# Performance work log

Measured on AMD Instinct MI355X. Metric: run time of the kernel, lower is better.

The kernel has to match this reference:

```python
import jax, jax.numpy as jnp
import numpy as np

TEMP = 0.05
EPS_SOFTMAX = 1e-6
EPS_LOG = 1e-6


def setup_inputs() -> dict:
    key = jax.random.key(0)
    k1, k2, k3, k4, k5 = jax.random.split(key, 5)
    B, F, N, C = 256, 128, 200000, 1000
    inputs = jax.random.normal(k1, (B, F), dtype=jnp.float32)
    inputs_s = jax.random.normal(k2, (B, F), dtype=jnp.float32)
    features = jax.random.normal(k3, (N, F), dtype=jnp.float32)
    # memory banks are kept L2-normalized (see MB.backward renorm)
    features = features / jnp.linalg.norm(features, axis=1, keepdims=True)
    labels = jax.random.randint(k4, (N,), 0, C, dtype=jnp.int64)
    indexes = jax.random.randint(k5, (B,), 0, N, dtype=jnp.int64)
    return {"inputs": inputs, "inputs_s": inputs_s, "features": features,
            "labels": labels, "indexes": indexes, "k": 10, "num_classes": C}


def reference(inputs, inputs_s, features, labels, indexes, k, num_classes):
    B = inputs.shape[0]
    N = features.shape[0]
    # features is a buffer (no grad in torch); MB backward also treats it as constant
    feats = jax.lax.stop_gradient(features)

    # MB.forward: inputs @ features.T, then /temp  -> [B, N]
    inputs_out = (inputs @ feats.T) / TEMP

    # local similarity [B, B]
    local = inputs @ inputs_s.T
    # topk neighbors in the bank, gather + per-sample bmm, sum over k -> [B, 1]
    _, nb_idx = jax.lax.top_k(inputs_out, k)          # [B, k]
    nb_ftr = feats[nb_idx]                             # [B, k, F]
    _local = jnp.einsum('bf,bkf->b', inputs, nb_ftr)[:, None]  # [B, 1]
    # (local + _local) masked to diagonal, then /temp
    local = (local + _local) * jnp.eye(B, dtype=local.dtype)
    local = local / TEMP

    targets = labels[indexes]                          # [B]

    # label-bucketed segment reductions -> sim [C, B]
    sim = jax.ops.segment_sum(inputs_out.T, labels, num_segments=num_classes)
    sim = sim + jax.ops.segment_sum(local, targets, num_segments=num_classes)

    nums = jax.ops.segment_sum(jnp.ones((N, 1), jnp.float32), labels,
                               num_segments=num_classes)        # [C, 1]
    nums_help = jax.ops.segment_sum(jnp.ones((B, 1), jnp.float32), targets,
                                    num_segments=num_classes)   # [C, 1]
    nums = nums + (nums_help > 0).astype(jnp.float32) * (k + 1)

    mask = (nums > 0).astype(jnp.float32)              # [C, 1]
    sim = sim / (mask * nums + (1.0 - mask))           # broadcast over B

    # masked softmax over classes, per sample: vec [B, C], mask [1, C]
    vec = sim.T
    m = mask.T                                          # [1, C]
    exps = jnp.exp(vec) * m
    masked_sim = exps / (jnp.sum(exps, axis=1, keepdims=True) + EPS_SOFTMAX)

    logp = jnp.log(masked_sim + EPS_LOG)
    loss = -jnp.mean(logp[jnp.arange(B), targets])
    return loss
```

## Files before the change

### kernel.cpp

```cpp
#include <hip/hip_runtime.h>

#define CMAX 1024
#define BQ 256
#define FQ 128
#define TN 64
#define QCAP 128
#define NBLK_DEF 768

typedef __attribute__((ext_vector_type(8))) short bf16x8;
typedef __attribute__((ext_vector_type(4))) float f32x4;

__device__ __forceinline__ unsigned short f2bf(float f){
  unsigned u = __float_as_uint(f);
  unsigned r = (u + 0x7FFFu + ((u >> 16) & 1u)) >> 16;
  return (unsigned short)r;
}
__device__ __forceinline__ unsigned encf(float f){
  unsigned u = __float_as_uint(f);
  return (u & 0x80000000u) ? ~u : (u | 0x80000000u);
}
__device__ __forceinline__ void ins16(float (&d)[16], float v){
  #pragma unroll
  for (int j = 15; j > 0; --j) d[j] = fminf(d[j-1], fmaxf(v, d[j]));
  d[0] = fmaxf(v, d[0]);
}

__global__ void k_prep(const float* __restrict__ inputs, const float* __restrict__ inputs_s,
                       const int* __restrict__ labels, const int* __restrict__ indexes,
                       unsigned short* __restrict__ inputs_bf,
                       int* __restrict__ cnt, int* __restrict__ numsh,
                       int* __restrict__ targets, float* __restrict__ diag,
                       float* __restrict__ thr, int N)
{
  __shared__ int h[CMAX];
  int t = threadIdx.x;
  for (int c = t; c < CMAX; c += 256) h[c] = 0;
  __syncthreads();
  int idx = blockIdx.x*256 + t;
  int stride = gridDim.x*256;
  for (int n = idx; n < N; n += stride) atomicAdd(&h[labels[n]], 1);
  for (int i = idx; i < BQ*FQ; i += stride) inputs_bf[i] = f2bf(inputs[i]);
  __syncthreads();
  for (int c = t; c < CMAX; c += 256){
    int v = h[c];
    if (v) atomicAdd(&cnt[c], v);
  }
  if (blockIdx.x == 0 && t < BQ){
    int tg = labels[indexes[t]];
    targets[t] = tg;
    atomicAdd(&numsh[tg], 1);
    float s = 0.f, s2 = 0.f;
    const float4* a = (const float4*)(inputs + t*FQ);
    const float4* b = (const float4*)(inputs_s + t*FQ);
    #pragma unroll
    for (int f = 0; f < FQ/4; ++f){
      float4 x = a[f], y = b[f];
      s  += x.x*y.x + x.y*y.y + x.z*y.z + x.w*y.w;
      s2 += x.x*x.x + x.y*x.y + x.z*x.z + x.w*x.w;
    }
    diag[t] = s;
    thr[t] = 3.05f * sqrtf(s2 * (1.0f/128.0f));
  }
}

__global__ void k_scan(const int* __restrict__ cnt, int* __restrict__ cur,
                       int* __restrict__ pstart, const int* __restrict__ cptr)
{
  __shared__ int s[CMAX];
  int C = cptr[0]; if (C > CMAX) C = CMAX;
  int t = threadIdx.x;
  s[t] = (t < C) ? cnt[t] : 0;
  __syncthreads();
  for (int off = 1; off < CMAX; off <<= 1){
    int v = s[t] + ((t >= off) ? s[t - off] : 0);
    __syncthreads();
    s[t] = v;
    __syncthreads();
  }
  if (t < C){
    int e = s[t] - cnt[t];
    cur[t] = e;
    pstart[t] = e;
  }
  if (t == C-1) pstart[C] = s[t];
}

__global__ void k_scatter(const int* __restrict__ labels, int* __restrict__ cur,
                          int* __restrict__ sorted_idx, int* __restrict__ sorted_cls, int N)
{
  int idx = blockIdx.x*blockDim.x + threadIdx.x;
  int stride = gridDim.x*blockDim.x;
  for (int n = idx; n < N; n += stride){
    int c = labels[n];
    int pos = atomicAdd(&cur[c], 1);
    sorted_idx[pos] = n;
    sorted_cls[pos] = c;
  }
}

__global__ __launch_bounds__(256, 3) void k_main(
    const float* __restrict__ feats,
    const int* __restrict__ sorted_idx,
    const int* __restrict__ sorted_cls,
    const unsigned short* __restrict__ inputs_bf,
    const float* __restrict__ thr,
    const int* __restrict__ pstart,
    float* __restrict__ sim,
    float* __restrict__ topk_ws,
    const int* __restrict__ cptr,
    int N, int nblk)
{
  __shared__ unsigned short fl[TN*FQ];
  __shared__ unsigned q_lds[4][QCAP];
  __shared__ int qn_lds[4];

  const int t = threadIdx.x;
  const int lane = t & 63;
  const int w = t >> 6;
  const int c16 = lane & 15;
  const int g = lane >> 4;
  const int g4 = g * 4;
  const int b0 = w * 64;
  const int rowoff = t >> 2;
  const int q = t & 3;

  float d[16];
  #pragma unroll
  for (int i2 = 0; i2 < 16; ++i2) d[i2] = -INFINITY;

  int C = cptr[0]; if (C > CMAX) C = CMAX;
  const int j = blockIdx.x;
  const int Tj  = (int)(((long long)j * N) / nblk);
  const int Tj1 = (int)(((long long)(j+1) * N) / nblk);
  int lo = 0, hi = C;
  while (lo < hi){ int mid = (lo+hi)>>1; if (pstart[mid] < Tj) lo = mid+1; else hi = mid; }
  const int c_lo = lo;
  hi = C;
  while (lo < hi){ int mid = (lo+hi)>>1; if (pstart[mid] < Tj1) lo = mid+1; else hi = mid; }
  const int c_hi = lo;
  const int e_lo = pstart[c_lo];
  const int e_hi = pstart[c_hi];

  if (e_lo < e_hi){
    float thrs[4];
    #pragma unroll
    for (int bt = 0; bt < 4; ++bt) thrs[bt] = thr[b0 + bt*16 + c16];
    float racc[4] = {0.f, 0.f, 0.f, 0.f};
    if (lane == 0) qn_lds[w] = 0;

    const int nch = (e_hi - e_lo + TN - 1) / TN;

    int myrow = e_lo + rowoff;
    int idx_cur = (myrow < e_hi) ? sorted_idx[myrow] : 0;

    for (int m = 0; m < nch; ++m){
      const int base = e_lo + m*TN;
      const int valid = min(TN, e_hi - base);

      const int nxtrow = myrow + TN;
      const int idx_nxt = ((m + 1 < nch) && (nxtrow < e_hi)) ? sorted_idx[nxtrow] : 0;

      const int mypos = base + lane;
      const int myc  = (mypos < e_hi)     ? sorted_cls[mypos]     : -1;
      const int mync = (mypos + 1 < e_hi) ? sorted_cls[mypos + 1] : -2;

      {
        const bool live = (rowoff < valid);
        const float4* src = (const float4*)(feats + (size_t)idx_cur * FQ);
        #pragma unroll
        for (int jj = 0; jj < 8; ++jj){
          float4 v;
          if (live) v = src[jj*4 + q];
          else { v.x = 0.f; v.y = 0.f; v.z = 0.f; v.w = 0.f; }
          int h0 = (jj*16 + q*4) ^ ((rowoff & 7) << 3);
          ushort4 u;
          u.x = f2bf(v.x); u.y = f2bf(v.y); u.z = f2bf(v.z); u.w = f2bf(v.w);
          *(ushort4*)&fl[rowoff*FQ + h0] = u;
        }
      }
      const unsigned long long bmask = __ballot((lane < valid) && (myc != mync));
      __syncthreads();

      f32x4 acc[4][4];
      #pragma unroll
      for (int nt = 0; nt < 4; ++nt)
        #pragma unroll
        for (int bt = 0; bt < 4; ++bt)
          acc[nt][bt] = (f32x4){0.f, 0.f, 0.f, 0.f};
      #pragma unroll
      for (int ks = 0; ks < 4; ++ks){
        bf16x8 af[4], bfr[4];
        #pragma unroll
        for (int nt = 0; nt < 4; ++nt){
          int r = nt*16 + c16;
          int h = r*FQ + ((ks*32 + g*8) ^ ((r & 7) << 3));
          af[nt] = *(const bf16x8*)&fl[h];
        }
        #pragma unroll
        for (int bt = 0; bt < 4; ++bt){
          int b = b0 + bt*16 + c16;
          bfr[bt] = *(const bf16x8*)&inputs_bf[b*FQ + ks*32 + g*8];
        }
        #pragma unroll
        for (int nt = 0; nt < 4; ++nt)
          #pragma unroll
          for (int bt = 0; bt < 4; ++bt)
            acc[nt][bt] = __builtin_amdgcn_mfma_f32_16x16x32_bf16(af[nt], bfr[bt], acc[nt][bt], 0, 0, 0);
      }

      #pragma unroll
      for (int bt = 0; bt < 4; ++bt){
        float smax = -INFINITY;
        #pragma unroll
        for (int nt = 0; nt < 4; ++nt)
          #pragma unroll
          for (int r = 0; r < 4; ++r)
            smax = fmaxf(smax, acc[nt][bt][r]);
        if (__any(smax > thrs[bt])){
          if (smax > thrs[bt]){
            #pragma unroll
            for (int nt = 0; nt < 4; ++nt)
              #pragma unroll
              for (int r = 0; r < 4; ++r){
                float v = acc[nt][bt][r];
                if (v > thrs[bt]){
                  int pos = atomicAdd(&qn_lds[w], 1);
                  if (pos < QCAP)
                    q_lds[w][pos] = (__float_as_uint(v) & 0xFFFFFF00u) | (unsigned)(bt*16 + c16);
                }
              }
          }
        }
      }

      if (bmask == 0ull){
        #pragma unroll
        for (int bt = 0; bt < 4; ++bt){
          float ss = 0.f;
          #pragma unroll
          for (int nt = 0; nt < 4; ++nt)
            #pragma unroll
            for (int r = 0; r < 4; ++r)
              ss += acc[nt][bt][r];
          ss += __shfl_xor(ss, 16, 64);
          ss += __shfl_xor(ss, 32, 64);
          racc[bt] += ss;
        }
      } else {
        int seglo = 0;
        unsigned long long mm = bmask;
        while (mm){
          const int p = (int)__builtin_ctzll(mm);
          float s4[4];
          #pragma unroll
          for (int bt = 0; bt < 4; ++bt){
            float ss = 0.f;
            #pragma unroll
            for (int nt = 0; nt < 4; ++nt)
              #pragma unroll
              for (int r = 0; r < 4; ++r){
                int n = nt*16 + g4 + r;
                ss += ((n >= seglo) && (n <= p)) ? acc[nt][bt][r] : 0.f;
              }
            ss += __shfl_xor(ss, 16, 64);
            ss += __shfl_xor(ss, 32, 64);
            if (seglo == 0) ss += racc[bt];
            s4[bt] = ss;
          }
          const int c = __shfl(myc, p, 64);
          if (g == 0){
            #pragma unroll
            for (int bt = 0; bt < 4; ++bt)
              sim[(size_t)c*BQ + b0 + bt*16 + c16] = s4[bt];
          }
          seglo = p + 1;
          mm &= mm - 1;
        }
        #pragma unroll
        for (int bt = 0; bt < 4; ++bt){
          float ss = 0.f;
          #pragma unroll
          for (int nt = 0; nt < 4; ++nt)
            #pragma unroll
            for (int r = 0; r < 4; ++r){
              int n = nt*16 + g4 + r;
              ss += (n >= seglo) ? acc[nt][bt][r] : 0.f;
            }
          ss += __shfl_xor(ss, 16, 64);
          ss += __shfl_xor(ss, 32, 64);
          racc[bt] = ss;
        }
      }

      __builtin_amdgcn_wave_barrier();
      asm volatile("s_waitcnt lgkmcnt(0)" ::: "memory");
      int qn = qn_lds[w];
      if (qn > QCAP) qn = QCAP;
      for (int qi = 0; qi < qn; ++qi){
        unsigned pk = q_lds[w][qi];
        if ((int)(pk & 0xFFu) == lane){
          float v = __uint_as_float(pk & 0xFFFFFF00u);
          if (v > d[15]) ins16(d, v);
        }
      }
      __builtin_amdgcn_wave_barrier();
      if (lane == 0) qn_lds[w] = 0;

      idx_cur = idx_nxt;
      myrow = nxtrow;
      __syncthreads();
    }
  }

  #pragma unroll
  for (int i2 = 0; i2 < 16; ++i2)
    topk_ws[((size_t)blockIdx.x*BQ + t)*16 + i2] = d[i2];
}

__global__ void k_merge(const float* __restrict__ topk_ws, int NB,
                        const float* __restrict__ diag, const int* __restrict__ targets,
                        float* __restrict__ sim, const int* __restrict__ kptr)
{
  __shared__ float Ld[4][64][16];
  const int t = threadIdx.x;
  const int lane = t & 63;
  const int w = t >> 6;
  const int b = blockIdx.x*4 + w;

  float d[16];
  #pragma unroll
  for (int j = 0; j < 16; ++j) d[j] = -INFINITY;
  for (int bk = lane; bk < NB; bk += 64){
    const float* src = topk_ws + ((size_t)bk*BQ + b)*16;
    for (int j = 0; j < 16; ++j){
      float v = src[j];
      if (!(v > d[15])) break;
      ins16(d, v);
    }
  }
  #pragma unroll
  for (int j = 0; j < 16; ++j) Ld[w][lane][j] = d[j];
  __syncthreads();
  int kk = kptr[0]; if (kk > 16) kk = 16;
  int h = 0;
  float myhead = Ld[w][lane][0];
  float tops = 0.f;
  for (int p = 0; p < 16; ++p){
    unsigned pk = (encf(myhead) & 0xFFFFFFC0u) | (unsigned)lane;
    #pragma unroll
    for (int s = 32; s > 0; s >>= 1){
      unsigned o = (unsigned)__shfl_xor((int)pk, s, 64);
      pk = (o > pk) ? o : pk;
    }
    int wl = (int)(pk & 63u);
    float val = __shfl(myhead, wl, 64);
    if (p < kk) tops += val;
    if (lane == wl){
      ++h;
      myhead = (h < 16) ? Ld[w][lane][h] : -INFINITY;
    }
  }
  if (lane == 0){
    atomicAdd(&sim[(size_t)targets[b]*BQ + b], diag[b] + tops);
  }
}

__global__ void k_expsum(const float* __restrict__ sim, const int* __restrict__ cnt,
                         const int* __restrict__ numsh, const int* __restrict__ targets,
                         const int* __restrict__ kptr, const int* __restrict__ cptr,
                         float* __restrict__ esum, float* __restrict__ etgt)
{
  int t = threadIdx.x;
  int C = cptr[0]; if (C > CMAX) C = CMAX;
  int kk = kptr[0];
  int tgt = targets[t];
  float local = 0.f;
  const float invT = 20.0f;
  for (int c = blockIdx.x; c < C; c += gridDim.x){
    float nums = (float)cnt[c] + ((numsh[c] > 0) ? (float)(kk + 1) : 0.f);
    float denom = (nums > 0.f) ? nums : 1.f;
    float val = sim[(size_t)c*BQ + t] * invT / denom;
    float e = (nums > 0.f) ? expf(val) : 0.f;
    local += e;
    if (c == tgt) etgt[t] = e;
  }
  atomicAdd(&esum[t], local);
}

__global__ void k_loss(const float* __restrict__ esum, const float* __restrict__ etgt,
                       float* __restrict__ out)
{
  __shared__ float red[BQ];
  int t = threadIdx.x;
  float p = etgt[t] / (esum[t] + 1e-6f);
  float l = -logf(p + 1e-6f);
  red[t] = l;
  __syncthreads();
  for (int off = 128; off > 0; off >>= 1){
    if (t < off) red[t] += red[t + off];
    __syncthreads();
  }
  if (t == 0) out[0] = red[0] / 256.0f;
}

extern "C" void kernel_launch(void* const* d_in, const int* in_sizes, int n_in,
                              void* d_out, int out_size, void* d_ws, size_t ws_size,
                              hipStream_t stream) {
  const float* inputs   = (const float*)d_in[0];
  const float* inputs_s = (const float*)d_in[1];
  const float* feats    = (const float*)d_in[2];
  const int*   labels   = (const int*)d_in[3];
  const int*   indexes  = (const int*)d_in[4];
  const int*   kptr     = (const int*)d_in[5];
  const int*   cptr     = (const int*)d_in[6];
  const int N = in_sizes[3];

  char* ws = (char*)d_ws;
  int*      cnt       = (int*)(ws + 0);
  int*      numsh     = (int*)(ws + 4096);
  float*    esum      = (float*)(ws + 8192);
  float*    etgt      = (float*)(ws + 9216);
  int*      targets   = (int*)(ws + 10240);
  float*    diag      = (float*)(ws + 11264);
  float*    thr       = (float*)(ws + 12288);
  int*      cur       = (int*)(ws + 13312);
  int*      pstart    = (int*)(ws + 17408);
  unsigned short* inputs_bf = (unsigned short*)(ws + 21760);
  float*    sim       = (float*)(ws + 87296);
  int*      sorted_idx = (int*)(ws + 1135872);
  int*      sorted_cls = sorted_idx + N;
  size_t off_topk = (1135872 + 8*(size_t)N + 255) & ~(size_t)255;
  float*    topk      = (float*)(ws + off_topk);

  int nblk = NBLK_DEF;
  long long topk_cap = ((long long)ws_size - (long long)off_topk) / (BQ*16*4);
  if (topk_cap < nblk) nblk = (int)topk_cap;
  if (nblk < 1) nblk = 1;
  int gN = (N + 255) / 256; if (gN > 128) gN = 128; if (gN < 1) gN = 1;

  hipMemsetAsync(ws, 0, 10240, stream);
  k_prep<<<64, 256, 0, stream>>>(inputs, inputs_s, labels, indexes, inputs_bf,
                                 cnt, numsh, targets, diag, thr, N);
  k_scan<<<1, 1024, 0, stream>>>(cnt, cur, pstart, cptr);
  k_scatter<<<gN, 256, 0, stream>>>(labels, cur, sorted_idx, sorted_cls, N);
  k_main<<<nblk, 256, 0, stream>>>(feats, sorted_idx, sorted_cls, inputs_bf, thr,
                                   pstart, sim, topk, cptr, N, nblk);
  k_merge<<<BQ/4, 256, 0, stream>>>(topk, nblk, diag, targets, sim, kptr);
  k_expsum<<<64, 256, 0, stream>>>(sim, cnt, numsh, targets, kptr, cptr, esum, etgt);
  k_loss<<<1, 256, 0, stream>>>(esum, etgt, (float*)d_out);
}
```

Measured before the change: 213.3 us.

## Stage gather indices in LDS and defer top-k queue drain to kernel end

Sorted indices and class IDs for each 64-row chunk are now loaded once into shared memory, with the next chunk prefetched into registers. The feature gather is remapped so 32 threads cover one row with coalesced float4 loads, instead of 4 threads per row. The per-chunk top-k candidate queue drain is removed, and candidates accumulate across all chunks in a queue enlarged from 128 to 512 entries, drained once at the end. This cuts per-iteration serial work but uses more LDS, which may lower occupancy, and risks silently dropping candidates if the queue overflows.

```diff
diff --git a/kernel.cpp b/kernel.cpp
--- a/kernel.cpp
+++ b/kernel.cpp
@@ -4,7 +4,7 @@
 #define BQ 256
 #define FQ 128
 #define TN 64
-#define QCAP 128
+#define QCAP 512
 #define NBLK_DEF 768
 
 typedef __attribute__((ext_vector_type(8))) short bf16x8;
@@ -111,6 +111,8 @@
     int N, int nblk)
 {
   __shared__ unsigned short fl[TN*FQ];
+  __shared__ int idx_s[TN];
+  __shared__ int cls_s[TN + 1];
   __shared__ unsigned q_lds[4][QCAP];
   __shared__ int qn_lds[4];
 
@@ -121,12 +123,10 @@
   const int g = lane >> 4;
   const int g4 = g * 4;
   const int b0 = w * 64;
-  const int rowoff = t >> 2;
-  const int q = t & 3;
-
-  float d[16];
-  #pragma unroll
-  for (int i2 = 0; i2 < 16; ++i2) d[i2] = -INFINITY;
+  const int rbase = t >> 5;
+  const int f4 = t & 31;
+
+  if (lane == 0) qn_lds[w] = 0;
 
   int C = cptr[0]; if (C > CMAX) C = CMAX;
   const int j = blockIdx.x;
@@ -146,40 +146,53 @@
     #pragma unroll
     for (int bt = 0; bt < 4; ++bt) thrs[bt] = thr[b0 + bt*16 + c16];
     float racc[4] = {0.f, 0.f, 0.f, 0.f};
-    if (lane == 0) qn_lds[w] = 0;
 
     const int nch = (e_hi - e_lo + TN - 1) / TN;
 
-    int myrow = e_lo + rowoff;
-    int idx_cur = (myrow < e_hi) ? sorted_idx[myrow] : 0;
+    if (t < TN + 1){
+      int pos = e_lo + t;
+      if (t < TN) idx_s[t] = (pos < e_hi) ? sorted_idx[pos] : 0;
+      cls_s[t] = (pos < e_hi) ? sorted_cls[pos] : -2;
+    }
+    __syncthreads();
 
     for (int m = 0; m < nch; ++m){
       const int base = e_lo + m*TN;
       const int valid = min(TN, e_hi - base);
 
-      const int nxtrow = myrow + TN;
-      const int idx_nxt = ((m + 1 < nch) && (nxtrow < e_hi)) ? sorted_idx[nxtrow] : 0;
-
-      const int mypos = base + lane;
-      const int myc  = (mypos < e_hi)     ? sorted_cls[mypos]     : -1;
-      const int mync = (mypos + 1 < e_hi) ? sorted_cls[mypos + 1] : -2;
+      int ireg = 0, creg = -2;
+      if (t < TN + 1){
+        int pos = base + TN + t;
+        if (pos < e_hi){
+          if (t < TN) ireg = sorted_idx[pos];
+          creg = sorted_cls[pos];
+        }
+      }
+      const int myc  = cls_s[lane];
+      const int mync = cls_s[lane + 1];
+      const unsigned long long bmask = __ballot((lane < valid) && (myc != mync));
 
       {
-        const bool live = (rowoff < valid);
-        const float4* src = (const float4*)(feats + (size_t)idx_cur * FQ);
+        const int h0 = (f4*4) ^ (rbase << 3);
         #pragma unroll
         for (int jj = 0; jj < 8; ++jj){
+          const int r = jj*8 + rbase;
           float4 v;
-          if (live) v = src[jj*4 + q];
-          else { v.x = 0.f; v.y = 0.f; v.z = 0.f; v.w = 0.f; }
-          int h0 = (jj*16 + q*4) ^ ((rowoff & 7) << 3);
+          if (r < valid){
+            const int gi = idx_s[r];
+            v = *(const float4*)(feats + (size_t)gi*FQ + f4*4);
+          } else { v.x = 0.f; v.y = 0.f; v.z = 0.f; v.w = 0.f; }
           ushort4 u;
           u.x = f2bf(v.x); u.y = f2bf(v.y); u.z = f2bf(v.z); u.w = f2bf(v.w);
-          *(ushort4*)&fl[rowoff*FQ + h0] = u;
-        }
-      }
-      const unsigned long long bmask = __ballot((lane < valid) && (myc != mync));
+          *(ushort4*)&fl[r*FQ + h0] = u;
+        }
+      }
       __syncthreads();
+
+      if (m + 1 < nch && t < TN + 1){
+        if (t < TN) idx_s[t] = ireg;
+        cls_s[t] = creg;
+      }
 
       f32x4 acc[4][4];
       #pragma unroll
@@ -193,8 +206,8 @@
         #pragma unroll
         for (int nt = 0; nt < 4; ++nt){
           int r = nt*16 + c16;
-          int h = r*FQ + ((ks*32 + g*8) ^ ((r & 7) << 3));
-          af[nt] = *(const bf16x8*)&fl[h];
+          int h2 = r*FQ + ((ks*32 + g*8) ^ ((r & 7) << 3));
+          af[nt] = *(const bf16x8*)&fl[h2];
         }
         #pragma unroll
         for (int bt = 0; bt < 4; ++bt){
@@ -216,20 +229,18 @@
           #pragma unroll
           for (int r = 0; r < 4; ++r)
             smax = fmaxf(smax, acc[nt][bt][r]);
-        if (__any(smax > thrs[bt])){
-          if (smax > thrs[bt]){
+        if (smax > thrs[bt]){
+          #pragma unroll
+          for (int nt = 0; nt < 4; ++nt)
             #pragma unroll
-            for (int nt = 0; nt < 4; ++nt)
-              #pragma unroll
-              for (int r = 0; r < 4; ++r){
-                float v = acc[nt][bt][r];
-                if (v > thrs[bt]){
-                  int pos = atomicAdd(&qn_lds[w], 1);
-                  if (pos < QCAP)
-                    q_lds[w][pos] = (__float_as_uint(v) & 0xFFFFFF00u) | (unsigned)(bt*16 + c16);
-                }
+            for (int r = 0; r < 4; ++r){
+              float v = acc[nt][bt][r];
+              if (v > thrs[bt]){
+                int pos = atomicAdd(&qn_lds[w], 1);
+                if (pos < QCAP)
+                  q_lds[w][pos] = (__float_as_uint(v) & 0xFFFFFF00u) | (unsigned)(bt*16 + c16);
               }
-          }
+            }
         }
       }
 
@@ -292,26 +303,25 @@
         }
       }
 
-      __builtin_amdgcn_wave_barrier();
-      asm volatile("s_waitcnt lgkmcnt(0)" ::: "memory");
-      int qn = qn_lds[w];
-      if (qn > QCAP) qn = QCAP;
-      for (int qi = 0; qi < qn; ++qi){
-        unsigned pk = q_lds[w][qi];
-        if ((int)(pk & 0xFFu) == lane){
-          float v = __uint_as_float(pk & 0xFFFFFF00u);
-          if (v > d[15]) ins16(d, v);
-        }
-      }
-      __builtin_amdgcn_wave_barrier();
-      if (lane == 0) qn_lds[w] = 0;
-
-      idx_cur = idx_nxt;
-      myrow = nxtrow;
       __syncthreads();
     }
   }
 
+  __builtin_amdgcn_wave_barrier();
+  asm volatile("s_waitcnt lgkmcnt(0)" ::: "memory");
+  __builtin_amdgcn_sched_barrier(0);
+  float d[16];
+  #pragma unroll
+  for (int i2 = 0; i2 < 16; ++i2) d[i2] = -INFINITY;
+  int qn = qn_lds[w];
+  if (qn > QCAP) qn = QCAP;
+  for (int qi = 0; qi < qn; ++qi){
+    unsigned pk = q_lds[w][qi];
+    if ((int)(pk & 0xFFu) == lane){
+      float v = __uint_as_float(pk & 0xFFFFFF00u);
+      if (v > d[15]) ins16(d, v);
+    }
+  }
   #pragma unroll
   for (int i2 = 0; i2 < 16; ++i2)
     topk_ws[((size_t)blockIdx.x*BQ + t)*16 + i2] = d[i2];
```

Result: faster. 204.8 us (-4.0%).

## Split block row range across waves, drop LDS staging and per-chunk barriers

Applied to the files above, without the earlier changes.

Each of the four waves now owns a quarter of the block's sorted row range and processes 32 rows at a time against all 256 batch columns. Feature rows are loaded straight from global memory into MFMA A-fragments, so the shared-memory tile and the two block barriers per chunk are gone. Class segments that may be shared with other waves or blocks are accumulated into sim with atomics, which requires zeroing the whole sim buffer with a larger memset. The top-k candidate queue grows and is merged once at kernel end. The trade-off is that each wave reloads the full inputs fragment for every 32-row step, and atomics plus a larger memset are added; a queue overflow could now drop candidates.

```diff
diff --git a/kernel.cpp b/kernel.cpp
--- a/kernel.cpp
+++ b/kernel.cpp
@@ -3,8 +3,8 @@
 #define CMAX 1024
 #define BQ 256
 #define FQ 128
-#define TN 64
-#define QCAP 128
+#define ROWS 32
+#define QCAP 512
 #define NBLK_DEF 768
 
 typedef __attribute__((ext_vector_type(8))) short bf16x8;
@@ -110,7 +110,6 @@
     const int* __restrict__ cptr,
     int N, int nblk)
 {
-  __shared__ unsigned short fl[TN*FQ];
   __shared__ unsigned q_lds[4][QCAP];
   __shared__ int qn_lds[4];
 
@@ -120,13 +119,9 @@
   const int c16 = lane & 15;
   const int g = lane >> 4;
   const int g4 = g * 4;
-  const int b0 = w * 64;
-  const int rowoff = t >> 2;
-  const int q = t & 3;
-
-  float d[16];
-  #pragma unroll
-  for (int i2 = 0; i2 < 16; ++i2) d[i2] = -INFINITY;
+  const int l32 = lane & 31;
+
+  if (lane == 0) qn_lds[w] = 0;
 
   int C = cptr[0]; if (C > CMAX) C = CMAX;
   const int j = blockIdx.x;
@@ -141,177 +136,186 @@
   const int e_lo = pstart[c_lo];
   const int e_hi = pstart[c_hi];
 
-  if (e_lo < e_hi){
-    float thrs[4];
+  const int span = e_hi - e_lo;
+  const int per = (span + 3) >> 2;
+  const int ws_ = e_lo + w * per;
+  const int we_ = min(ws_ + per, e_hi);
+
+  if (ws_ < we_){
+    float racc[16];
     #pragma unroll
-    for (int bt = 0; bt < 4; ++bt) thrs[bt] = thr[b0 + bt*16 + c16];
-    float racc[4] = {0.f, 0.f, 0.f, 0.f};
-    if (lane == 0) qn_lds[w] = 0;
-
-    const int nch = (e_hi - e_lo + TN - 1) / TN;
-
-    int myrow = e_lo + rowoff;
-    int idx_cur = (myrow < e_hi) ? sorted_idx[myrow] : 0;
-
-    for (int m = 0; m < nch; ++m){
-      const int base = e_lo + m*TN;
-      const int valid = min(TN, e_hi - base);
-
-      const int nxtrow = myrow + TN;
-      const int idx_nxt = ((m + 1 < nch) && (nxtrow < e_hi)) ? sorted_idx[nxtrow] : 0;
-
-      const int mypos = base + lane;
-      const int myc  = (mypos < e_hi)     ? sorted_cls[mypos]     : -1;
-      const int mync = (mypos + 1 < e_hi) ? sorted_cls[mypos + 1] : -2;
-
-      {
-        const bool live = (rowoff < valid);
-        const float4* src = (const float4*)(feats + (size_t)idx_cur * FQ);
+    for (int i2 = 0; i2 < 16; ++i2) racc[i2] = 0.f;
+
+    for (int base = ws_; base < we_; base += ROWS){
+      const int valid = min(ROWS, we_ - base);
+
+      const int i0 = (c16      < valid) ? sorted_idx[base + c16]      : -1;
+      const int i1 = (16 + c16 < valid) ? sorted_idx[base + 16 + c16] : -1;
+
+      int cls_a = -1, cls_b = -9;
+      if (l32 < valid){
+        int rl = base + l32;
+        cls_a = sorted_cls[rl];
+        cls_b = (rl + 1 < N) ? sorted_cls[rl + 1] : -9;
+      }
+      unsigned bmask = (unsigned)__ballot((lane < 32) && (l32 < valid) && (cls_a != cls_b));
+      if (valid < 32) bmask &= ((1u << valid) - 1u);
+
+      bf16x8 af[2][4];
+      #pragma unroll
+      for (int m = 0; m < 2; ++m){
+        const int im = (m == 0) ? i0 : i1;
+        const float* rp = feats + (size_t)((im >= 0) ? im : 0) * FQ;
         #pragma unroll
-        for (int jj = 0; jj < 8; ++jj){
-          float4 v;
-          if (live) v = src[jj*4 + q];
-          else { v.x = 0.f; v.y = 0.f; v.z = 0.f; v.w = 0.f; }
-          int h0 = (jj*16 + q*4) ^ ((rowoff & 7) << 3);
-          ushort4 u;
-          u.x = f2bf(v.x); u.y = f2bf(v.y); u.z = f2bf(v.z); u.w = f2bf(v.w);
-          *(ushort4*)&fl[rowoff*FQ + h0] = u;
+        for (int ks = 0; ks < 4; ++ks){
+          float4 va, vb;
+          if (im >= 0){
+            va = *(const float4*)(rp + ks*32 + g*8);
+            vb = *(const float4*)(rp + ks*32 + g*8 + 4);
+          } else {
+            va.x=va.y=va.z=va.w=0.f; vb.x=vb.y=vb.z=vb.w=0.f;
+          }
+          bf16x8 a;
+          a[0]=(short)f2bf(va.x); a[1]=(short)f2bf(va.y);
+          a[2]=(short)f2bf(va.z); a[3]=(short)f2bf(va.w);
+          a[4]=(short)f2bf(vb.x); a[5]=(short)f2bf(vb.y);
+          a[6]=(short)f2bf(vb.z); a[7]=(short)f2bf(vb.w);
+          af[m][ks] = a;
         }
       }
-      const unsigned long long bmask = __ballot((lane < valid) && (myc != mync));
-      __syncthreads();
-
-      f32x4 acc[4][4];
+
       #pragma unroll
-      for (int nt = 0; nt < 4; ++nt)
+      for (int q = 0; q < 4; ++q){
+        f32x4 acc[2][4];
         #pragma unroll
-        for (int bt = 0; bt < 4; ++bt)
-          acc[nt][bt] = (f32x4){0.f, 0.f, 0.f, 0.f};
-      #pragma unroll
-      for (int ks = 0; ks < 4; ++ks){
-        bf16x8 af[4], bfr[4];
+        for (int m = 0; m < 2; ++m)
+          #pragma unroll
+          for (int nt = 0; nt < 4; ++nt)
+            acc[m][nt] = (f32x4){0.f,0.f,0.f,0.f};
+
+        #pragma unroll
+        for (int ks = 0; ks < 4; ++ks){
+          #pragma unroll
+          for (int nt = 0; nt < 4; ++nt){
+            const int b = q*64 + nt*16 + c16;
+            bf16x8 bfr = *(const bf16x8*)&inputs_bf[(size_t)b*FQ + ks*32 + g*8];
+            acc[0][nt] = __builtin_amdgcn_mfma_f32_16x16x32_bf16(af[0][ks], bfr, acc[0][nt], 0,0,0);
+            acc[1][nt] = __builtin_amdgcn_mfma_f32_16x16x32_bf16(af[1][ks], bfr, acc[1][nt], 0,0,0);
+          }
+        }
+
         #pragma unroll
         for (int nt = 0; nt < 4; ++nt){
-          int r = nt*16 + c16;
-          int h = r*FQ + ((ks*32 + g*8) ^ ((r & 7) << 3));
-          af[nt] = *(const bf16x8*)&fl[h];
-        }
-        #pragma unroll
-        for (int bt = 0; bt < 4; ++bt){
-          int b = b0 + bt*16 + c16;
-          bfr[bt] = *(const bf16x8*)&inputs_bf[b*FQ + ks*32 + g*8];
-        }
-        #pragma unroll
-        for (int nt = 0; nt < 4; ++nt)
+          const int b = q*64 + nt*16 + c16;
+          const float thrq = thr[b];
+          float smax = -INFINITY;
           #pragma unroll
-          for (int bt = 0; bt < 4; ++bt)
-            acc[nt][bt] = __builtin_amdgcn_mfma_f32_16x16x32_bf16(af[nt], bfr[bt], acc[nt][bt], 0, 0, 0);
-      }
-
-      #pragma unroll
-      for (int bt = 0; bt < 4; ++bt){
-        float smax = -INFINITY;
-        #pragma unroll
-        for (int nt = 0; nt < 4; ++nt)
-          #pragma unroll
-          for (int r = 0; r < 4; ++r)
-            smax = fmaxf(smax, acc[nt][bt][r]);
-        if (__any(smax > thrs[bt])){
-          if (smax > thrs[bt]){
+          for (int m = 0; m < 2; ++m)
             #pragma unroll
-            for (int nt = 0; nt < 4; ++nt)
+            for (int r = 0; r < 4; ++r)
+              smax = fmaxf(smax, acc[m][nt][r]);
+          if (smax > thrq){
+            #pragma unroll
+            for (int m = 0; m < 2; ++m)
               #pragma unroll
               for (int r = 0; r < 4; ++r){
-                float v = acc[nt][bt][r];
-                if (v > thrs[bt]){
+                float v = acc[m][nt][r];
+                if (v > thrq){
                   int pos = atomicAdd(&qn_lds[w], 1);
                   if (pos < QCAP)
-                    q_lds[w][pos] = (__float_as_uint(v) & 0xFFFFFF00u) | (unsigned)(bt*16 + c16);
+                    q_lds[w][pos] = (__float_as_uint(v) & 0xFFFFFF00u) | (unsigned)b;
                 }
               }
           }
         }
-      }
-
-      if (bmask == 0ull){
-        #pragma unroll
-        for (int bt = 0; bt < 4; ++bt){
-          float ss = 0.f;
+
+        if (bmask == 0u){
           #pragma unroll
-          for (int nt = 0; nt < 4; ++nt)
-            #pragma unroll
-            for (int r = 0; r < 4; ++r)
-              ss += acc[nt][bt][r];
-          ss += __shfl_xor(ss, 16, 64);
-          ss += __shfl_xor(ss, 32, 64);
-          racc[bt] += ss;
-        }
-      } else {
-        int seglo = 0;
-        unsigned long long mm = bmask;
-        while (mm){
-          const int p = (int)__builtin_ctzll(mm);
-          float s4[4];
-          #pragma unroll
-          for (int bt = 0; bt < 4; ++bt){
+          for (int nt = 0; nt < 4; ++nt){
             float ss = 0.f;
             #pragma unroll
-            for (int nt = 0; nt < 4; ++nt)
+            for (int m = 0; m < 2; ++m)
+              #pragma unroll
+              for (int r = 0; r < 4; ++r)
+                ss += acc[m][nt][r];
+            ss += __shfl_xor(ss, 16, 64);
+            ss += __shfl_xor(ss, 32, 64);
+            racc[q*4 + nt] += ss;
+          }
+        } else {
+          int seglo = 0;
+          unsigned mm = bmask;
+          while (mm){
+            const int p = (int)__builtin_ctz(mm);
+            const int c = __shfl(cls_a, p, 64);
+            const bool shared = (pstart[c] < ws_) || (pstart[c+1] > we_);
+            #pragma unroll
+            for (int nt = 0; nt < 4; ++nt){
+              float ss = 0.f;
+              #pragma unroll
+              for (int m = 0; m < 2; ++m)
+                #pragma unroll
+                for (int r = 0; r < 4; ++r){
+                  int rr = m*16 + g4 + r;
+                  ss += ((rr >= seglo) && (rr <= p)) ? acc[m][nt][r] : 0.f;
+                }
+              ss += __shfl_xor(ss, 16, 64);
+              ss += __shfl_xor(ss, 32, 64);
+              if (seglo == 0) ss += racc[q*4 + nt];
+              if (g == 0){
+                float* dst = &sim[(size_t)c*BQ + q*64 + nt*16 + c16];
+                if (shared) atomicAdd(dst, ss);
+                else        *dst = ss;
+              }
+            }
+            seglo = p + 1;
+            mm &= mm - 1;
+          }
+          #pragma unroll
+          for (int nt = 0; nt < 4; ++nt){
+            float ss = 0.f;
+            #pragma unroll
+            for (int m = 0; m < 2; ++m)
               #pragma unroll
               for (int r = 0; r < 4; ++r){
-                int n = nt*16 + g4 + r;
-                ss += ((n >= seglo) && (n <= p)) ? acc[nt][bt][r] : 0.f;
+                int rr = m*16 + g4 + r;
+                ss += (rr >= seglo) ? acc[m][nt][r] : 0.f;
               }
             ss += __shfl_xor(ss, 16, 64);
             ss += __shfl_xor(ss, 32, 64);
-            if (seglo == 0) ss += racc[bt];
-            s4[bt] = ss;
-          }
-          const int c = __shfl(myc, p, 64);
-          if (g == 0){
-            #pragma unroll
-            for (int bt = 0; bt < 4; ++bt)
-              sim[(size_t)c*BQ + b0 + bt*16 + c16] = s4[bt];
-          }
-          seglo = p + 1;
-          mm &= mm - 1;
-        }
-        #pragma unroll
-        for (int bt = 0; bt < 4; ++bt){
-          float ss = 0.f;
-          #pragma unroll
-          for (int nt = 0; nt < 4; ++nt)
-            #pragma unroll
-            for (int r = 0; r < 4; ++r){
-              int n = nt*16 + g4 + r;
-              ss += (n >= seglo) ? acc[nt][bt][r] : 0.f;
-            }
-          ss += __shfl_xor(ss, 16, 64);
-          ss += __shfl_xor(ss, 32, 64);
-          racc[bt] = ss;
+            racc[q*4 + nt] = ss;
+          }
         }
       }
-
-      __builtin_amdgcn_wave_barrier();
-      asm volatile("s_waitcnt lgkmcnt(0)" ::: "memory");
-      int qn = qn_lds[w];
-      if (qn > QCAP) qn = QCAP;
-      for (int qi = 0; qi < qn; ++qi){
-        unsigned pk = q_lds[w][qi];
-        if ((int)(pk & 0xFFu) == lane){
-          float v = __uint_as_float(pk & 0xFFFFFF00u);
-          if (v > d[15]) ins16(d, v);
-        }
+    }
+
+    const int c_last = sorted_cls[we_ - 1];
+    if (g == 0){
+      #pragma unroll
+      for (int q = 0; q < 4; ++q)
+        #pragma unroll
+        for (int nt = 0; nt < 4; ++nt)
+          atomicAdd(&sim[(size_t)c_last*BQ + q*64 + nt*16 + c16], racc[q*4 + nt]);
+    }
+  }
+
+  __syncthreads();
+
+  float d[16];
+  #pragma unroll
+  for (int i2 = 0; i2 < 16; ++i2) d[i2] = -INFINITY;
+  #pragma unroll
+  for (int wq = 0; wq < 4; ++wq){
+    int qn = qn_lds[wq];
+    if (qn > QCAP) qn = QCAP;
+    for (int qi = 0; qi < qn; ++qi){
+      unsigned pk = q_lds[wq][qi];
+      if ((int)(pk & 0xFFu) == t){
+        float v = __uint_as_float(pk & 0xFFFFFF00u);
+        if (v > d[15]) ins16(d, v);
       }
-      __builtin_amdgcn_wave_barrier();
-      if (lane == 0) qn_lds[w] = 0;
-
-      idx_cur = idx_nxt;
-      myrow = nxtrow;
-      __syncthreads();
-    }
-  }
-
+    }
+  }
   #pragma unroll
   for (int i2 = 0; i2 < 16; ++i2)
     topk_ws[((size_t)blockIdx.x*BQ + t)*16 + i2] = d[i2];
@@ -420,13 +424,13 @@
   int*      numsh     = (int*)(ws + 4096);
   float*    esum      = (float*)(ws + 8192);
   float*    etgt      = (float*)(ws + 9216);
-  int*      targets   = (int*)(ws + 10240);
-  float*    diag      = (float*)(ws + 11264);
-  float*    thr       = (float*)(ws + 12288);
-  int*      cur       = (int*)(ws + 13312);
-  int*      pstart    = (int*)(ws + 17408);
-  unsigned short* inputs_bf = (unsigned short*)(ws + 21760);
-  float*    sim       = (float*)(ws + 87296);
+  float*    sim       = (float*)(ws + 10240);
+  int*      targets   = (int*)(ws + 1058816);
+  float*    diag      = (float*)(ws + 1059840);
+  float*    thr       = (float*)(ws + 1060864);
+  int*      cur       = (int*)(ws + 1061888);
+  int*      pstart    = (int*)(ws + 1065984);
+  unsigned short* inputs_bf = (unsigned short*)(ws + 1070336);
   int*      sorted_idx = (int*)(ws + 1135872);
   int*      sorted_cls = sorted_idx + N;
   size_t off_topk = (1135872 + 8*(size_t)N + 255) & ~(size_t)255;
@@ -438,7 +442,7 @@
   if (nblk < 1) nblk = 1;
   int gN = (N + 255) / 256; if (gN > 128) gN = 128; if (gN < 1) gN = 1;
 
-  hipMemsetAsync(ws, 0, 10240, stream);
+  hipMemsetAsync(ws, 0, 1058816, stream);
   k_prep<<<64, 256, 0, stream>>>(inputs, inputs_s, labels, indexes, inputs_bf,
                                  cnt, numsh, targets, diag, thr, N);
   k_scan<<<1, 1024, 0, stream>>>(cnt, cur, pstart, cptr);
```

New measurement: 301.0 us. 1.41x slower.
